# Kernel optimization log

Measured on AMD Instinct MI355X. Metric: run time of the kernel, lower is better.

The kernel has to match this reference:

```python
import jax, jax.numpy as jnp
import numpy as np

HIDDEN = 1024
NUM_EXPERTS = 8
TOP_K = 2
BATCH, SEQ = 4, 4096


def setup_inputs() -> dict:
    key = jax.random.key(0)
    ks = jax.random.split(key, 7)
    s = 0.02
    x = jax.random.normal(ks[0], (BATCH, SEQ, HIDDEN), dtype=jnp.float32)
    router_w = jax.random.normal(ks[1], (HIDDEN, NUM_EXPERTS), dtype=jnp.float32) * s
    router_b = jnp.zeros((NUM_EXPERTS,), dtype=jnp.float32)
    w1 = jax.random.normal(ks[2], (NUM_EXPERTS, HIDDEN, 2 * HIDDEN), dtype=jnp.float32) * s
    b1 = jnp.zeros((NUM_EXPERTS, 2 * HIDDEN), dtype=jnp.float32)
    w2 = jax.random.normal(ks[3], (NUM_EXPERTS, 2 * HIDDEN, HIDDEN), dtype=jnp.float32) * s
    b2 = jnp.zeros((NUM_EXPERTS, HIDDEN), dtype=jnp.float32)
    return {"x": x, "router_w": router_w, "router_b": router_b,
            "w1": w1, "b1": b1, "w2": w2, "b2": b2}


def reference(x, router_w, router_b, w1, b1, w2, b2):
    # Router: softmax over experts, then top-k and renormalize.
    logits = jnp.einsum("bsh,he->bse", x, router_w) + router_b        # [B,S,E]
    probs = jax.nn.softmax(logits, axis=-1)
    topk_p, topk_i = jax.lax.top_k(probs, TOP_K)                       # [B,S,K]
    topk_p = topk_p / jnp.sum(topk_p, axis=-1, keepdims=True)

    out = jnp.zeros_like(x)
    for e in range(NUM_EXPERTS):
        # combine weight for this expert (0 for tokens that didn't route here;
        # top_k indices are distinct so at most one slot matches)
        w = jnp.sum(jnp.where(topk_i == e, topk_p, 0.0), axis=-1)      # [B,S]
        h = jax.nn.relu(jnp.einsum("bsh,hf->bsf", x, w1[e]) + b1[e])   # [B,S,2H]
        y = jnp.einsum("bsf,fh->bsh", h, w2[e]) + b2[e]                # [B,S,H]
        out = out + w[..., None] * y
    return out
```

## Files before the change

### kernel.cpp

```cpp
#include <hip/hip_runtime.h>

#define HIDDEN 1024
#define FF 2048
#define NEXP 8
#define NTOK 16384
#define NPAIR (2 * NTOK)
#define MAXT 264

typedef short short8 __attribute__((ext_vector_type(8)));
typedef unsigned short ushort4v __attribute__((ext_vector_type(4)));
typedef float f32x4 __attribute__((ext_vector_type(4)));

__device__ __forceinline__ unsigned short f2b(float f) {
  union { float f; unsigned int u; } v; v.f = f;
  unsigned int u = v.u;
  return (unsigned short)((u + 0x7fffu + ((u >> 16) & 1u)) >> 16);
}
__device__ __forceinline__ float b2f(unsigned short b) {
  union { unsigned int u; float f; } v; v.u = ((unsigned int)b) << 16;
  return v.f;
}

__device__ __forceinline__ void gload16(const unsigned short* g, unsigned short* l) {
  __builtin_amdgcn_global_load_lds(
      (const __attribute__((address_space(1))) unsigned int*)g,
      (__attribute__((address_space(3))) unsigned int*)l,
      16, 0, 0);
}

#define PIPE_WAIT(n) do { \
    asm volatile("s_waitcnt vmcnt(" #n ")" ::: "memory"); \
    __builtin_amdgcn_sched_barrier(0); \
  } while (0)
#define ABAR do { \
    asm volatile("s_barrier" ::: "memory"); \
    __builtin_amdgcn_sched_barrier(0); \
  } while (0)

#define W2T_OFF 0ull
#define W1T_OFF (W2T_OFF + (unsigned long long)NEXP * HIDDEN * FF * 2)
#define XB_OFF  (W1T_OFF + (unsigned long long)NEXP * FF * HIDDEN * 2)
#define H_OFF   (XB_OFF + (unsigned long long)NTOK * HIDDEN * 2)
#define CNT_OFF (H_OFF + (unsigned long long)NPAIR * FF * 2)
#define PLIST_OFF (CNT_OFF + 256ull)
#define PW_OFF    (PLIST_OFF + (unsigned long long)NEXP * NTOK * 4)
#define TOPS_OFF  (PW_OFF + (unsigned long long)NPAIR * 4)
#define W0_OFF    (TOPS_OFF + (unsigned long long)NTOK * 4)
#define WQ_OFF    (W0_OFF + (unsigned long long)NTOK * 4)
#define YP_OFF    W1T_OFF
#define WS_NEED   (WQ_OFF + 4096ull)

__global__ void zero_out_k(float4* __restrict__ out) {
  out[(size_t)blockIdx.x * 256 + threadIdx.x] = float4{0.f, 0.f, 0.f, 0.f};
}

__global__ void transpose_cast_k(const float* __restrict__ in,
                                 unsigned short* __restrict__ out,
                                 int R, int C) {
  __shared__ float tile[32][33];
  const size_t eoff = (size_t)blockIdx.z * R * C;
  const float* inp = in + eoff;
  unsigned short* outp = out + eoff;
  const int c = threadIdx.x & 31;
  const int r0 = threadIdx.x >> 5;
  const int gr = blockIdx.y * 32, gc = blockIdx.x * 32;
#pragma unroll
  for (int i = 0; i < 4; i++) {
    int r = r0 + i * 8;
    tile[r][c] = inp[(size_t)(gr + r) * C + gc + c];
  }
  __syncthreads();
#pragma unroll
  for (int i = 0; i < 4; i++) {
    int r = r0 + i * 8;
    outp[(size_t)(gc + r) * R + gr + c] = f2b(tile[c][r]);
  }
}

__global__ void router_k(const float* __restrict__ x, const float* __restrict__ rw,
                         const float* __restrict__ rb, int* __restrict__ tops,
                         float* __restrict__ w0f, unsigned short* __restrict__ xb,
                         int* __restrict__ cnt) {
  if (blockIdx.x == 0 && threadIdx.x < NEXP) cnt[threadIdx.x] = 0;
  const int wid = threadIdx.x >> 6;
  const int lane = threadIdx.x & 63;
  const int t = blockIdx.x * 4 + wid;
  const float* xr = x + (size_t)t * HIDDEN;
  float acc[8];
#pragma unroll
  for (int e = 0; e < 8; e++) acc[e] = 0.f;
#pragma unroll
  for (int i = 0; i < 16; i++) {
    int hh = lane + 64 * i;
    float xv = xr[hh];
    const float4* rwp = reinterpret_cast<const float4*>(rw + (size_t)hh * 8);
    float4 a = rwp[0], b = rwp[1];
    acc[0] += xv * a.x; acc[1] += xv * a.y; acc[2] += xv * a.z; acc[3] += xv * a.w;
    acc[4] += xv * b.x; acc[5] += xv * b.y; acc[6] += xv * b.z; acc[7] += xv * b.w;
  }
  {
    const float4* xr4 = reinterpret_cast<const float4*>(xr);
    unsigned short* xbr = xb + (size_t)t * HIDDEN;
#pragma unroll
    for (int i = 0; i < 4; i++) {
      float4 f = xr4[lane + 64 * i];
      ushort4v o;
      o[0] = f2b(f.x); o[1] = f2b(f.y); o[2] = f2b(f.z); o[3] = f2b(f.w);
      *reinterpret_cast<ushort4v*>(&xbr[(lane + 64 * i) * 4]) = o;
    }
  }
#pragma unroll
  for (int off = 32; off; off >>= 1) {
#pragma unroll
    for (int e = 0; e < 8; e++) acc[e] += __shfl_xor(acc[e], off);
  }
  if (lane == 0) {
#pragma unroll
    for (int e = 0; e < 8; e++) acc[e] += rb[e];
    int i0 = 0; float m0 = acc[0];
#pragma unroll
    for (int e = 1; e < 8; e++) if (acc[e] > m0) { m0 = acc[e]; i0 = e; }
    int i1 = -1; float m1 = -1e30f;
#pragma unroll
    for (int e = 0; e < 8; e++) if (e != i0 && acc[e] > m1) { m1 = acc[e]; i1 = e; }
    float w0 = 1.f / (1.f + __expf(m1 - m0));
    tops[t] = i0 | (i1 << 4);
    w0f[t] = w0;
  }
}

__global__ __launch_bounds__(256)
void scatter_k(const int* __restrict__ tops, const float* __restrict__ w0f,
               int* __restrict__ cnt, int* __restrict__ plist, float* __restrict__ pw) {
  __shared__ int lcnt[NEXP];
  __shared__ int lbase[NEXP];
  const int tid = threadIdx.x;
  const int t = blockIdx.x * 256 + tid;
  if (tid < NEXP) lcnt[tid] = 0;
  __syncthreads();
  const int packed = tops[t];
  const int i0 = packed & 15, i1 = packed >> 4;
  const float w0 = w0f[t];
  const int s0 = atomicAdd(&lcnt[i0], 1);
  const int s1 = atomicAdd(&lcnt[i1], 1);
  __syncthreads();
  if (tid < NEXP) lbase[tid] = atomicAdd(&cnt[tid], lcnt[tid]);
  __syncthreads();
  plist[i0 * NTOK + lbase[i0] + s0] = 2 * t;
  plist[i1 * NTOK + lbase[i1] + s1] = 2 * t + 1;
  pw[2 * t] = w0;
  pw[2 * t + 1] = 1.f - w0;
}

__global__ void plan_k(const int* __restrict__ cnt, int* __restrict__ workq) {
  if (threadIdx.x == 0) {
    int idx = 0;
    for (int e = 0; e < NEXP; e++) {
      int nt = (cnt[e] + 127) >> 7;
      for (int m = 0; m < nt; m++) workq[idx++] = (e << 16) | m;
    }
    while (idx < MAXT) workq[idx++] = -1;
  }
}

__global__ __launch_bounds__(256)
void combine_k(const unsigned short* __restrict__ ypair, const float* __restrict__ pw,
               float* __restrict__ out) {
  const int t = blockIdx.x * 2 + (threadIdx.x >> 7);
  const int i = (threadIdx.x & 127) * 8;
  const float w0 = pw[2 * t], w1 = pw[2 * t + 1];
  const short8 y0 = *(const short8*)&ypair[(size_t)(2 * t) * HIDDEN + i];
  const short8 y1 = *(const short8*)&ypair[(size_t)(2 * t + 1) * HIDDEN + i];
  float* orow = out + (size_t)t * HIDDEN + i;
#pragma unroll
  for (int j = 0; j < 8; j++)
    orow[j] = w0 * b2f((unsigned short)y0[j]) + w1 * b2f((unsigned short)y1[j]);
}

template <int PHASE, int YP>
__global__ __launch_bounds__(256, 3)
void ffn_k(const unsigned short* __restrict__ xb, const unsigned short* __restrict__ wT,
           const float* __restrict__ bias, const unsigned short* __restrict__ hin,
           unsigned short* __restrict__ hout, float* __restrict__ out,
           const int* __restrict__ cnt, const int* __restrict__ plist,
           const float* __restrict__ pw, const int* __restrict__ workq) {
  constexpr int K = (PHASE == 1) ? HIDDEN : FF;
  constexpr int N = (PHASE == 1) ? FF : HIDDEN;
  constexpr int NT = K / 32;
  constexpr int NTN = N / 128;
  constexpr int NWG = MAXT * NTN;

  constexpr int q8 = NWG / 8, r8 = NWG % 8;
  const int bid = blockIdx.x;
  const int xcd = bid & 7, idx = bid >> 3;
  const int wgid = (xcd < r8 ? xcd * (q8 + 1) : r8 * (q8 + 1) + (xcd - r8) * q8) + idx;
  const int mt = wgid / NTN;
  const int n0g = (wgid % NTN) * 128;

  const int w = workq[mt];
  if (w < 0) return;
  const int e = w >> 16;
  const int m0g = (w & 0xffff) * 128;
  const int mcnt = cnt[e];
  const int mrem = mcnt - m0g;

  __shared__ alignas(16) unsigned short As[3][128][32];
  __shared__ alignas(16) unsigned short Bs[3][128][32];
  __shared__ int rowpair[128];

  const int tid = threadIdx.x;
  if (tid < 128) rowpair[tid] = (tid < mrem) ? plist[e * NTOK + m0g + tid] : -1;
  __syncthreads();

  const int wid = tid >> 6;
  const int lane = tid & 63;

  const int sslot = (lane & 3) ^ ((lane >> 2) & 3);
  const int rsub = lane >> 2;
  const unsigned short* wTe = wT + (size_t)e * N * K;

  const unsigned short* gA[2];
  const unsigned short* gB[2];
#pragma unroll
  for (int i = 0; i < 2; i++) {
    const int c = wid + i * 4;
    const int row = c * 16 + rsub;
    int p = rowpair[row];
    if (p < 0) p = 0;
    const unsigned short* abase;
    if constexpr (PHASE == 1) abase = xb + (size_t)(p >> 1) * HIDDEN;
    else                      abase = hin + (size_t)p * FF;
    gA[i] = abase + sslot * 8;
    gB[i] = wTe + (size_t)(n0g + row) * K + sslot * 8;
  }

  const int wr = (wid >> 1) * 64;
  const int wc = (wid & 1) * 64;
  const int fr = lane & 15;
  const int fg = lane >> 4;
  const int fsw = (fr & 3);

  f32x4 acc[4][4];
#pragma unroll
  for (int i = 0; i < 4; i++)
#pragma unroll
    for (int j = 0; j < 4; j++) acc[i][j] = f32x4{0.f, 0.f, 0.f, 0.f};

#pragma unroll
  for (int b = 0; b < 3; b++) {
#pragma unroll
    for (int i = 0; i < 2; i++) {
      const int c = wid + i * 4;
      gload16(gA[i] + b * 32, &As[b][c * 16][0]);
      gload16(gB[i] + b * 32, &Bs[b][c * 16][0]);
    }
  }

  int cur = 0;
  for (int t = 0; t < NT; ++t) {
    if (t < NT - 2)       PIPE_WAIT(8);
    else if (t == NT - 2) PIPE_WAIT(4);
    else                  PIPE_WAIT(0);
    ABAR;

    short8 af[4], bf[4];
#pragma unroll
    for (int mi = 0; mi < 4; mi++)
      af[mi] = *(const short8*)&As[cur][wr + mi * 16 + fr][(fg ^ fsw) * 8];
#pragma unroll
    for (int ni = 0; ni < 4; ni++)
      bf[ni] = *(const short8*)&Bs[cur][wc + ni * 16 + fr][(fg ^ fsw) * 8];
#pragma unroll
    for (int mi = 0; mi < 4; mi++)
#pragma unroll
      for (int ni = 0; ni < 4; ni++)
        acc[mi][ni] = __builtin_amdgcn_mfma_f32_16x16x32_bf16(af[mi], bf[ni], acc[mi][ni], 0, 0, 0);

    ABAR;

    if (t + 3 < NT) {
      const int kt = (t + 3) * 32;
#pragma unroll
      for (int i = 0; i < 2; i++) {
        const int c = wid + i * 4;
        gload16(gA[i] + kt, &As[cur][c * 16][0]);
        gload16(gB[i] + kt, &Bs[cur][c * 16][0]);
      }
    }
    cur = (cur == 2) ? 0 : cur + 1;
  }

  float bv[4];
#pragma unroll
  for (int ni = 0; ni < 4; ni++) bv[ni] = bias[(size_t)e * N + n0g + wc + ni * 16 + fr];

#pragma unroll
  for (int mi = 0; mi < 4; mi++) {
#pragma unroll
    for (int r = 0; r < 4; r++) {
      int m = wr + mi * 16 + fg * 4 + r;
      if (m >= mrem) continue;
      int p = rowpair[m];
      if constexpr (PHASE == 1) {
        unsigned short* hr = hout + (size_t)p * FF + n0g;
#pragma unroll
        for (int ni = 0; ni < 4; ni++) {
          float v = acc[mi][ni][r] + bv[ni];
          hr[wc + ni * 16 + fr] = f2b(fmaxf(v, 0.f));
        }
      } else if constexpr (YP == 1) {
        unsigned short* yr = hout + (size_t)p * HIDDEN + n0g;
#pragma unroll
        for (int ni = 0; ni < 4; ni++) {
          float v = acc[mi][ni][r] + bv[ni];
          yr[wc + ni * 16 + fr] = f2b(v);
        }
      } else {
        float wgt = pw[p];
        float* orow = out + (size_t)(p >> 1) * HIDDEN + n0g;
#pragma unroll
        for (int ni = 0; ni < 4; ni++) {
          float v = (acc[mi][ni][r] + bv[ni]) * wgt;
          atomicAdd(&orow[wc + ni * 16 + fr], v);
        }
      }
    }
  }
}

extern "C" void kernel_launch(void* const* d_in, const int* in_sizes, int n_in,
                              void* d_out, int out_size, void* d_ws, size_t ws_size,
                              hipStream_t stream) {
  const float* x  = (const float*)d_in[0];
  const float* rw = (const float*)d_in[1];
  const float* rb = (const float*)d_in[2];
  const float* w1 = (const float*)d_in[3];
  const float* b1 = (const float*)d_in[4];
  const float* w2 = (const float*)d_in[5];
  const float* b2 = (const float*)d_in[6];
  float* out = (float*)d_out;
  char* ws = (char*)d_ws;

  unsigned short* w2t = (unsigned short*)(ws + W2T_OFF);
  unsigned short* w1t = (unsigned short*)(ws + W1T_OFF);
  unsigned short* xb  = (unsigned short*)(ws + XB_OFF);
  unsigned short* h   = (unsigned short*)(ws + H_OFF);
  int* cnt   = (int*)(ws + CNT_OFF);
  int* plist = (int*)(ws + PLIST_OFF);
  float* pwt = (float*)(ws + PW_OFF);
  int* tops  = (int*)(ws + TOPS_OFF);
  float* w0f = (float*)(ws + W0_OFF);
  int* workq = (int*)(ws + WQ_OFF);
  unsigned short* ypair = (unsigned short*)(ws + YP_OFF);

  const bool use_yp = (ws_size >= WS_NEED);

  if (!use_yp)
    hipLaunchKernelGGL(zero_out_k, dim3(16384), dim3(256), 0, stream, (float4*)out);
  hipLaunchKernelGGL(transpose_cast_k, dim3(FF / 32, HIDDEN / 32, NEXP), dim3(256), 0, stream,
                     w1, w1t, HIDDEN, FF);
  hipLaunchKernelGGL(transpose_cast_k, dim3(HIDDEN / 32, FF / 32, NEXP), dim3(256), 0, stream,
                     w2, w2t, FF, HIDDEN);
  hipLaunchKernelGGL(router_k, dim3(NTOK / 4), dim3(256), 0, stream, x, rw, rb, tops, w0f, xb, cnt);
  hipLaunchKernelGGL(scatter_k, dim3(NTOK / 256), dim3(256), 0, stream, tops, w0f, cnt, plist, pwt);
  hipLaunchKernelGGL(plan_k, dim3(1), dim3(64), 0, stream, cnt, workq);
  hipLaunchKernelGGL((ffn_k<1, 0>), dim3(MAXT * (FF / 128)), dim3(256), 0, stream,
                     xb, w1t, b1, (const unsigned short*)nullptr, h, (float*)nullptr,
                     cnt, plist, pwt, workq);
  if (use_yp) {
    hipLaunchKernelGGL((ffn_k<2, 1>), dim3(MAXT * (HIDDEN / 128)), dim3(256), 0, stream,
                       xb, w2t, b2, h, ypair, (float*)nullptr,
                       cnt, plist, pwt, workq);
    hipLaunchKernelGGL(combine_k, dim3(NTOK / 2), dim3(256), 0, stream, ypair, pwt, out);
  } else {
    hipLaunchKernelGGL((ffn_k<2, 0>), dim3(MAXT * (HIDDEN / 128)), dim3(256), 0, stream,
                       xb, w2t, b2, h, (unsigned short*)nullptr, out,
                       cnt, plist, pwt, workq);
  }
}
```

Baseline: 465.8 us.

## Widen FFN GEMM tile to 128x256 with 512-thread blocks sharing A

```diff
diff --git a/kernel.cpp b/kernel.cpp
--- a/kernel.cpp
+++ b/kernel.cpp
@@ -178,7 +178,7 @@
 }
 
 template <int PHASE, int YP>
-__global__ __launch_bounds__(256, 3)
+__global__ __launch_bounds__(512, 4)
 void ffn_k(const unsigned short* __restrict__ xb, const unsigned short* __restrict__ wT,
            const float* __restrict__ bias, const unsigned short* __restrict__ hin,
            unsigned short* __restrict__ hout, float* __restrict__ out,
@@ -187,15 +187,14 @@
   constexpr int K = (PHASE == 1) ? HIDDEN : FF;
   constexpr int N = (PHASE == 1) ? FF : HIDDEN;
   constexpr int NT = K / 32;
-  constexpr int NTN = N / 128;
+  constexpr int NTN = N / 256;
   constexpr int NWG = MAXT * NTN;
 
-  constexpr int q8 = NWG / 8, r8 = NWG % 8;
+  constexpr int q8 = NWG / 8;
   const int bid = blockIdx.x;
-  const int xcd = bid & 7, idx = bid >> 3;
-  const int wgid = (xcd < r8 ? xcd * (q8 + 1) : r8 * (q8 + 1) + (xcd - r8) * q8) + idx;
+  const int wgid = (bid & 7) * q8 + (bid >> 3);
   const int mt = wgid / NTN;
-  const int n0g = (wgid % NTN) * 128;
+  const int n0g = (wgid % NTN) * 256;
 
   const int w = workq[mt];
   if (w < 0) return;
@@ -204,41 +203,44 @@
   const int mcnt = cnt[e];
   const int mrem = mcnt - m0g;
 
-  __shared__ alignas(16) unsigned short As[3][128][32];
-  __shared__ alignas(16) unsigned short Bs[3][128][32];
+  __shared__ alignas(16) unsigned short S[3][384][32];
   __shared__ int rowpair[128];
 
   const int tid = threadIdx.x;
   if (tid < 128) rowpair[tid] = (tid < mrem) ? plist[e * NTOK + m0g + tid] : -1;
   __syncthreads();
 
-  const int wid = tid >> 6;
+  const int w8 = tid >> 6;
   const int lane = tid & 63;
 
   const int sslot = (lane & 3) ^ ((lane >> 2) & 3);
   const int rsub = lane >> 2;
   const unsigned short* wTe = wT + (size_t)e * N * K;
 
-  const unsigned short* gA[2];
-  const unsigned short* gB[2];
-#pragma unroll
-  for (int i = 0; i < 2; i++) {
-    const int c = wid + i * 4;
-    const int row = c * 16 + rsub;
-    int p = rowpair[row];
-    if (p < 0) p = 0;
-    const unsigned short* abase;
-    if constexpr (PHASE == 1) abase = xb + (size_t)(p >> 1) * HIDDEN;
-    else                      abase = hin + (size_t)p * FF;
-    gA[i] = abase + sslot * 8;
-    gB[i] = wTe + (size_t)(n0g + row) * K + sslot * 8;
-  }
-
-  const int wr = (wid >> 1) * 64;
-  const int wc = (wid & 1) * 64;
+  const unsigned short* gS[3];
+  int ldsRow[3];
+#pragma unroll
+  for (int j = 0; j < 3; j++) {
+    const int gr = w8 * 48 + j * 16;
+    ldsRow[j] = gr;
+    const int r = gr + rsub;
+    if (gr < 128) {
+      int p = rowpair[r];
+      if (p < 0) p = 0;
+      const unsigned short* abase;
+      if constexpr (PHASE == 1) abase = xb + (size_t)(p >> 1) * HIDDEN;
+      else                      abase = hin + (size_t)p * FF;
+      gS[j] = abase + sslot * 8;
+    } else {
+      gS[j] = wTe + (size_t)(n0g + (r - 128)) * K + sslot * 8;
+    }
+  }
+
+  const int wr = (w8 >> 2) * 64;
+  const int wc = (w8 & 3) * 64;
   const int fr = lane & 15;
   const int fg = lane >> 4;
-  const int fsw = (fr & 3);
+  const int fsw = fr & 3;
 
   f32x4 acc[4][4];
 #pragma unroll
@@ -247,29 +249,25 @@
     for (int j = 0; j < 4; j++) acc[i][j] = f32x4{0.f, 0.f, 0.f, 0.f};
 
 #pragma unroll
-  for (int b = 0; b < 3; b++) {
-#pragma unroll
-    for (int i = 0; i < 2; i++) {
-      const int c = wid + i * 4;
-      gload16(gA[i] + b * 32, &As[b][c * 16][0]);
-      gload16(gB[i] + b * 32, &Bs[b][c * 16][0]);
-    }
-  }
+  for (int b = 0; b < 3; b++)
+#pragma unroll
+    for (int j = 0; j < 3; j++)
+      gload16(gS[j] + b * 32, &S[b][ldsRow[j]][0]);
 
   int cur = 0;
   for (int t = 0; t < NT; ++t) {
-    if (t < NT - 2)       PIPE_WAIT(8);
-    else if (t == NT - 2) PIPE_WAIT(4);
+    if (t < NT - 2)       PIPE_WAIT(6);
+    else if (t == NT - 2) PIPE_WAIT(3);
     else                  PIPE_WAIT(0);
     ABAR;
 
     short8 af[4], bf[4];
 #pragma unroll
     for (int mi = 0; mi < 4; mi++)
-      af[mi] = *(const short8*)&As[cur][wr + mi * 16 + fr][(fg ^ fsw) * 8];
+      af[mi] = *(const short8*)&S[cur][wr + mi * 16 + fr][(fg ^ fsw) * 8];
 #pragma unroll
     for (int ni = 0; ni < 4; ni++)
-      bf[ni] = *(const short8*)&Bs[cur][wc + ni * 16 + fr][(fg ^ fsw) * 8];
+      bf[ni] = *(const short8*)&S[cur][128 + wc + ni * 16 + fr][(fg ^ fsw) * 8];
 #pragma unroll
     for (int mi = 0; mi < 4; mi++)
 #pragma unroll
@@ -281,11 +279,8 @@
     if (t + 3 < NT) {
       const int kt = (t + 3) * 32;
 #pragma unroll
-      for (int i = 0; i < 2; i++) {
-        const int c = wid + i * 4;
-        gload16(gA[i] + kt, &As[cur][c * 16][0]);
-        gload16(gB[i] + kt, &Bs[cur][c * 16][0]);
-      }
+      for (int j = 0; j < 3; j++)
+        gload16(gS[j] + kt, &S[cur][ldsRow[j]][0]);
     }
     cur = (cur == 2) ? 0 : cur + 1;
   }
@@ -364,16 +359,16 @@
   hipLaunchKernelGGL(router_k, dim3(NTOK / 4), dim3(256), 0, stream, x, rw, rb, tops, w0f, xb, cnt);
   hipLaunchKernelGGL(scatter_k, dim3(NTOK / 256), dim3(256), 0, stream, tops, w0f, cnt, plist, pwt);
   hipLaunchKernelGGL(plan_k, dim3(1), dim3(64), 0, stream, cnt, workq);
-  hipLaunchKernelGGL((ffn_k<1, 0>), dim3(MAXT * (FF / 128)), dim3(256), 0, stream,
+  hipLaunchKernelGGL((ffn_k<1, 0>), dim3(MAXT * (FF / 256)), dim3(512), 0, stream,
                      xb, w1t, b1, (const unsigned short*)nullptr, h, (float*)nullptr,
                      cnt, plist, pwt, workq);
   if (use_yp) {
-    hipLaunchKernelGGL((ffn_k<2, 1>), dim3(MAXT * (HIDDEN / 128)), dim3(256), 0, stream,
+    hipLaunchKernelGGL((ffn_k<2, 1>), dim3(MAXT * (HIDDEN / 256)), dim3(512), 0, stream,
                        xb, w2t, b2, h, ypair, (float*)nullptr,
                        cnt, plist, pwt, workq);
     hipLaunchKernelGGL(combine_k, dim3(NTOK / 2), dim3(256), 0, stream, ypair, pwt, out);
   } else {
-    hipLaunchKernelGGL((ffn_k<2, 0>), dim3(MAXT * (HIDDEN / 128)), dim3(256), 0, stream,
+    hipLaunchKernelGGL((ffn_k<2, 0>), dim3(MAXT * (HIDDEN / 256)), dim3(512), 0, stream,
                        xb, w2t, b2, h, (unsigned short*)nullptr, out,
                        cnt, plist, pwt, workq);
   }
```

Result: no change. 467.7 us (median of 2 runs) (+0.4%).
